# Kernel optimization log

Measured on AMD Instinct MI355X. Metric: run time of the kernel, lower is better.

The kernel has to match this reference:

```python
import jax, jax.numpy as jnp
import numpy as np

NUM_CAT = 16
SEG_LENS = np.array([4, 2, 2, 4, 4, 3, 3, 2, 4, 6, 2, 6, 3, 3, 3, 3], dtype=np.int64)
SHIFTS = np.concatenate([[0], np.cumsum(SEG_LENS)[:-1]]).astype(np.int64)
MAX_SEG_COUNT = int(SEG_LENS.max())           # 6
MAX_SEG = int(SHIFTS[-1] + SEG_LENS[-1] - 1)  # 53
IN = 128
N = 65536
EPS = 1e-5  # BatchNorm1d default eps
SLOPE = 0.2  # LeakyReLU negative slope


def setup_inputs() -> dict:
    key = jax.random.key(0)
    ks = jax.random.split(key, 4)
    features = jax.random.normal(ks[0], (N, IN), dtype=jnp.float32)
    category_labels = jax.random.randint(ks[1], (N,), 0, NUM_CAT, dtype=jnp.int64)
    # channel raising MLP: Linear(IN -> NUM_CAT*IN, bias=False)
    W1 = jax.random.normal(ks[2], (IN, NUM_CAT * IN), dtype=jnp.float32) * (1.0 / np.sqrt(IN))
    gamma = jnp.ones((NUM_CAT * IN,), dtype=jnp.float32)
    beta = jnp.zeros((NUM_CAT * IN,), dtype=jnp.float32)
    # UnaryConv weight: xavier_normal over (NUM_CAT, IN, MAX_SEG_COUNT)
    W2 = jax.random.normal(ks[3], (NUM_CAT, IN, MAX_SEG_COUNT), dtype=jnp.float32) * np.sqrt(2.0 / (IN + MAX_SEG_COUNT))
    bias = jnp.zeros((MAX_SEG_COUNT,), dtype=jnp.float32)
    return dict(features=features, W1=W1, gamma=gamma, beta=beta, W2=W2, bias=bias,
                category_labels=category_labels)


def reference(features, W1, gamma, beta, W2, bias, category_labels):
    n = features.shape[0]
    # channel raising: Linear -> BatchNorm1d (batch stats) -> LeakyReLU(0.2)
    h = features @ W1                                   # [N, C*D]
    mean = h.mean(axis=0)
    var = h.var(axis=0)                                 # biased, as in torch BN
    h = (h - mean) / jnp.sqrt(var + EPS) * gamma + beta
    h = jnp.where(h >= 0, h, SLOPE * h)
    # per-category batched matmul classifier
    h = h.reshape(n, NUM_CAT, IN).transpose(1, 0, 2)    # [C, N, D]
    logits_all = jnp.einsum('cnd,cds->cns', h, W2) + bias  # [C, N, S]
    n_idx = jnp.arange(n)
    logits = logits_all[category_labels, n_idx]         # gather: [N, S]
    logsm = jax.nn.log_softmax(logits, axis=-1)
    # scatter into per-category segment ranges of the [N, MAX_SEG+1] output
    shifts = jnp.asarray(SHIFTS)[category_labels]       # [N]
    seg_len = jnp.asarray(SEG_LENS)[category_labels]    # [N]
    s_idx = jnp.arange(MAX_SEG_COUNT)
    valid = s_idx[None, :] < seg_len[:, None]           # [N, S]
    cols = jnp.clip(shifts[:, None] + s_idx[None, :], 0, MAX_SEG)
    vals = jnp.where(valid, logsm, 0.0)                 # invalid slots add 0
    out = jnp.zeros((n, MAX_SEG + 1), dtype=logsm.dtype)
    out = out.at[n_idx[:, None], cols].add(vals)
    return out
```

## Files before the change

### kernel.cpp

```cpp
#include <hip/hip_runtime.h>
#include <hip/hip_bf16.h>

#define NCAT 16

typedef __attribute__((ext_vector_type(8))) short short8v;
typedef __attribute__((ext_vector_type(4))) float float4v;
typedef __attribute__((ext_vector_type(16))) float f32x16;

__constant__ int c_shift[NCAT] = {0,4,6,8,12,16,19,22,24,28,34,36,42,45,48,51};
__constant__ int c_len[NCAT]   = {4,2,2,4,4,3,3,2,4,6,2,6,3,3,3,3};


static inline __device__ unsigned pk2(float lo, float hi) {
  float2 f2; f2.x = lo; f2.y = hi;
  __hip_bfloat162 h = __float22bfloat162_rn(f2);
  unsigned u; __builtin_memcpy(&u, &h, 4);
  return u;
}
static inline __device__ float bf2f(unsigned short v) {
  unsigned u = (unsigned)v << 16;
  float f; __builtin_memcpy(&f, &u, 4);
  return f;
}

template<bool PART>
__global__ __launch_bounds__(1024) void k_stats_m(
    const float* __restrict__ F, const float* __restrict__ W1,
    const float* __restrict__ W2,
    float* __restrict__ Gdst, unsigned* __restrict__ Gp16,
    float* __restrict__ sv, float* __restrict__ svpart,
    unsigned short* __restrict__ Wlb, float* __restrict__ W2p)
{
  const int tid = threadIdx.x;
  if (blockIdx.x >= 256) {
    const int cat = (int)blockIdx.x - 256;
    for (int e = tid; e < 2048; e += 1024) {
      const int fid = e >> 6, l = e & 63;
      const int ks = fid >> 3, ct = fid & 7;
      const int kb = 32 * ks + 8 * (l >> 4);
      const int c = cat * 128 + 16 * ct + (l & 15);
      uint4 pk;
      pk.x = pk2(W1[(size_t)(kb + 0) * 2048 + c], W1[(size_t)(kb + 1) * 2048 + c]);
      pk.y = pk2(W1[(size_t)(kb + 2) * 2048 + c], W1[(size_t)(kb + 3) * 2048 + c]);
      pk.z = pk2(W1[(size_t)(kb + 4) * 2048 + c], W1[(size_t)(kb + 5) * 2048 + c]);
      pk.w = pk2(W1[(size_t)(kb + 6) * 2048 + c], W1[(size_t)(kb + 7) * 2048 + c]);
      *(uint4*)(Wlb + ((size_t)(cat * 32 + fid) * 64 + l) * 8) = pk;
    }
    if (tid < 1024) {
      const int c = tid >> 3, s = tid & 7;
      W2p[cat * 1024 + tid] = (s < 6) ? W2[cat * 768 + c * 6 + s] : 0.f;
    }
    return;
  }

  const int rowbase = blockIdx.x * 256;
  const int wid = tid >> 6, lane = tid & 63;
  const int wi = wid >> 2, wj = wid & 3;
  const int i0 = wi * 32, j0 = wj * 32;
  const int lr = lane & 31, lh = lane >> 5;

  f32x16 acc;
  #pragma unroll
  for (int e = 0; e < 16; ++e) acc[e] = 0.f;
  float svacc = 0.f;

  for (int ch = 0; ch < 8; ++ch) {
    #pragma unroll
    for (int h = 0; h < 2; ++h) {
      const int rbase = rowbase + ch * 32 + 16 * h + 8 * lh;
      float fa[8], fb[8];
      #pragma unroll
      for (int j = 0; j < 8; ++j) {
        const float* rp = F + (size_t)(rbase + j) * 128;
        fa[j] = rp[i0 + lr];
        fb[j] = rp[j0 + lr];
      }
      if (wj == 0) {
        #pragma unroll
        for (int j = 0; j < 8; ++j) svacc += fa[j];
      }
      uint4 av4, bv4;
      av4.x = pk2(fa[0], fa[1]); av4.y = pk2(fa[2], fa[3]);
      av4.z = pk2(fa[4], fa[5]); av4.w = pk2(fa[6], fa[7]);
      bv4.x = pk2(fb[0], fb[1]); bv4.y = pk2(fb[2], fb[3]);
      bv4.z = pk2(fb[4], fb[5]); bv4.w = pk2(fb[6], fb[7]);
      acc = __builtin_amdgcn_mfma_f32_32x32x16_bf16(
          __builtin_bit_cast(short8v, av4), __builtin_bit_cast(short8v, bv4),
          acc, 0, 0, 0);
    }
  }

  if (wj == 0) {
    svacc += __shfl_xor(svacc, 32);
    if (lane < 32) {
      if (PART) svpart[blockIdx.x * 128 + i0 + lr] = svacc;
      else      atomicAdd(&sv[i0 + lr], svacc);
    }
  }

  if (PART) {
    unsigned* gp = Gp16 + (size_t)blockIdx.x * 8192;
    #pragma unroll
    for (int t = 0; t < 8; ++t) {
      const int rowe = ((2 * t) & 3) + 8 * (t >> 1) + 4 * lh;
      gp[((i0 + rowe) >> 1) * 128 + j0 + lr] = pk2(acc[2 * t], acc[2 * t + 1]);
    }
  } else {
    #pragma unroll
    for (int reg = 0; reg < 16; ++reg) {
      const int row = (reg & 3) + 8 * (reg >> 2) + 4 * lh;
      atomicAdd(&Gdst[(i0 + row) * 128 + j0 + lr], acc[reg]);
    }
  }
}

__global__ __launch_bounds__(256) void k_reduce(
    const unsigned* __restrict__ Gp16, const float* __restrict__ svpart,
    float* __restrict__ G, float* __restrict__ sv)
{
  const int b = blockIdx.x, tid = threadIdx.x;
  if (b < 64) {
    const int e = b * 128 + (tid >> 1);
    const int half = tid & 1;
    float lo = 0.f, hi = 0.f;
    #pragma unroll 4
    for (int p = half * 128; p < half * 128 + 128; ++p) {
      const unsigned u = Gp16[(size_t)p * 8192 + e];
      lo += bf2f((unsigned short)(u & 0xffffu));
      hi += bf2f((unsigned short)(u >> 16));
    }
    lo += __shfl_xor(lo, 1);
    hi += __shfl_xor(hi, 1);
    if (half == 0) {
      const int pr = e >> 7, col = e & 127;
      G[(2 * pr) * 128 + col]     = lo;
      G[(2 * pr + 1) * 128 + col] = hi;
    }
  } else {
    if (tid < 128) {
      float s = 0.f;
      #pragma unroll 8
      for (int p = 0; p < 256; ++p) s += svpart[p * 128 + tid];
      sv[tid] = s;
    }
  }
}

__global__ __launch_bounds__(256) void k_params(
    const float* __restrict__ G, const float* __restrict__ sv,
    const float* __restrict__ W1, const float* __restrict__ gamma,
    const float* __restrict__ beta, float* __restrict__ scale,
    float* __restrict__ shiftv)
{
  __shared__ float Gl[128][133];
  __shared__ float Wl[128][16];
  __shared__ float redq[16][16];
  __shared__ float redm[16][16];
  const int tid = threadIdx.x;
  const int jb = blockIdx.x * 16;
  for (int i = tid; i < 16384; i += 256) Gl[i >> 7][i & 127] = G[i];
  for (int i = tid; i < 2048; i += 256) {
    int k = i >> 4, col = i & 15;
    Wl[k][col] = W1[(size_t)k * 2048 + jb + col];
  }
  __syncthreads();
  const int col = tid & 15, part = tid >> 4;
  float msq = 0.f, mean = 0.f;
  for (int ii = 0; ii < 8; ++ii) {
    const int i = part * 8 + ii;
    const float wi = Wl[i][col];
    float inner = 0.f;
    #pragma unroll 8
    for (int k = 0; k < 128; ++k) inner = fmaf(Gl[i][k], Wl[k][col], inner);
    msq = fmaf(wi, inner, msq);
  }
  #pragma unroll
  for (int kk = 0; kk < 8; ++kk) {
    const int k = part * 8 + kk;
    mean = fmaf(sv[k], Wl[k][col], mean);
  }
  redq[part][col] = msq;
  redm[part][col] = mean;
  __syncthreads();
  if (tid < 16) {
    float q = 0.f, m = 0.f;
    #pragma unroll
    for (int p = 0; p < 16; ++p) { q += redq[p][tid]; m += redm[p][tid]; }
    m *= (1.f / 65536.f);
    q *= (1.f / 65536.f);
    float var = q - m * m;
    float sc = gamma[jb + tid] * rsqrtf(var + 1e-5f);
    scale[jb + tid] = sc;
    shiftv[jb + tid] = beta[jb + tid] - m * sc;
  }
}

__global__ __launch_bounds__(512, 2) void k_main(
    const float* __restrict__ F, const unsigned short* __restrict__ Wlb,
    const float* __restrict__ W2p, const float* __restrict__ bias,
    const float* __restrict__ scale, const float* __restrict__ shiftv,
    const int* __restrict__ lab, float* __restrict__ out)
{
  __shared__ __attribute__((aligned(16))) unsigned short Fl[128 * 128];
  __shared__ __attribute__((aligned(16))) float obuf[128 * 54];
  __shared__ unsigned short lrows[128];
  __shared__ int wcs[2][NCAT];
  __shared__ int loff[NCAT + 1];
  __shared__ unsigned char gcat[32], gsub[32];
  __shared__ int gtot;

  const int tid = threadIdx.x;
  const int blk = (int)blockIdx.x;
  const int wid = tid >> 6, lane = tid & 63;
  const int lrow = lane & 15, lhi = lane >> 4;

  {
    for (int i = tid; i < 2048; i += 512) {
      const int r = i >> 4, cb = i & 15;
      const float4* src = (const float4*)(F + ((size_t)(blk * 128 + r)) * 128 + cb * 8);
      const float4 a0 = src[0];
      const float4 a1 = src[1];
      uint4 pk;
      pk.x = pk2(a0.x, a0.y); pk.y = pk2(a0.z, a0.w);
      pk.z = pk2(a1.x, a1.y); pk.w = pk2(a1.z, a1.w);
      const int co = (cb * 16) ^ ((r & 7) << 4);
      *(uint4*)((char*)Fl + r * 256 + co) = pk;
    }
    float4* ob4 = (float4*)obuf;
    for (int i = tid; i < 1728; i += 512) ob4[i] = make_float4(0.f, 0.f, 0.f, 0.f);
  }

  int myc = 0, myrank = 0;
  if (tid < 128) {
    myc = lab[blk * 128 + tid];
    const unsigned long long lanebit = 1ull << lane;
    #pragma unroll
    for (int cc = 0; cc < NCAT; ++cc) {
      unsigned long long m = __ballot(myc == cc);
      if (lane == 0) wcs[wid][cc] = (int)__popcll(m);
      if (myc == cc) myrank = (int)__popcll(m & (lanebit - 1));
    }
  }
  __syncthreads();
  if (tid == 0) {
    int a = 0, g = 0;
    for (int c = 0; c < NCAT; ++c) {
      loff[c] = a;
      const int cnt = wcs[0][c] + wcs[1][c];
      for (int s2 = 0; s2 * 16 < cnt; ++s2) {
        gcat[g] = (unsigned char)c; gsub[g] = (unsigned char)s2; ++g;
      }
      a += cnt;
    }
    loff[NCAT] = a;
    gtot = g;
  }
  __syncthreads();
  if (tid < 128) {
    const int wbase = (wid == 1) ? wcs[0][myc] : 0;
    lrows[loff[myc] + wbase + myrank] = (unsigned short)tid;
  }
  __syncthreads();

  float bi[6];
  #pragma unroll
  for (int s = 0; s < 6; ++s) bi[s] = bias[s];

  const int ng = gtot;
  for (int g = wid; g < ng; g += 8) {
    const int cat = gcat[g];
    const int slot0 = loff[cat] + ((int)gsub[g] << 4);
    const int hi2 = loff[cat + 1];
    const int navail = min(16, hi2 - slot0);
    const int srow = lrows[min(slot0 + lrow, hi2 - 1)];
    const unsigned short* wbase2 = Wlb + (size_t)cat * 16384;

    float4v acc[8];
    #pragma unroll
    for (int ct = 0; ct < 8; ++ct) acc[ct] = (float4v){0.f, 0.f, 0.f, 0.f};

    #pragma unroll
    for (int ks = 0; ks < 4; ++ks) {
      const int co = (ks * 64 + lhi * 16) ^ ((srow & 7) << 4);
      const short8v av = *(const short8v*)((const char*)Fl + srow * 256 + co);
      #pragma unroll
      for (int ct = 0; ct < 8; ++ct) {
        short8v bv = *(const short8v*)(wbase2 + ((ks * 8 + ct) * 64 + lane) * 8);
        acc[ct] = __builtin_amdgcn_mfma_f32_16x16x32_bf16(av, bv, acc[ct], 0, 0, 0);
      }
    }

    float p[4][6];
    #pragma unroll
    for (int j = 0; j < 4; ++j)
      #pragma unroll
      for (int s = 0; s < 6; ++s) p[j][s] = 0.f;
    #pragma unroll
    for (int ct = 0; ct < 8; ++ct) {
      const int c = ct * 16 + lrow;
      const float s_ = scale[cat * 128 + c];
      const float h_ = shiftv[cat * 128 + c];
      const float4* w2p4 = (const float4*)(W2p + ((size_t)cat * 128 + c) * 8);
      const float4 wa = w2p4[0];
      const float4 wb = w2p4[1];
      const float w2v[6] = {wa.x, wa.y, wa.z, wa.w, wb.x, wb.y};
      #pragma unroll
      for (int j = 0; j < 4; ++j) {
        float a = acc[ct][j] * s_ + h_;
        a = (a >= 0.f) ? a : 0.2f * a;
        #pragma unroll
        for (int s = 0; s < 6; ++s) p[j][s] = fmaf(a, w2v[s], p[j][s]);
      }
    }
    const bool b1 = (lrow & 1) != 0;
    const bool b2 = (lrow & 2) != 0;
    float q[2][6], r[6];
    #pragma unroll
    for (int t = 0; t < 2; ++t)
      #pragma unroll
      for (int s = 0; s < 6; ++s) {
        float snd = b1 ? p[2 * t][s] : p[2 * t + 1][s];
        float kp  = b1 ? p[2 * t + 1][s] : p[2 * t][s];
        q[t][s] = kp + __shfl_xor(snd, 1);
      }
    #pragma unroll
    for (int s = 0; s < 6; ++s) {
      float snd = b2 ? q[0][s] : q[1][s];
      float kp  = b2 ? q[1][s] : q[0][s];
      r[s] = kp + __shfl_xor(snd, 2);
    }
    #pragma unroll
    for (int s = 0; s < 6; ++s) r[s] += __shfl_xor(r[s], 4);
    #pragma unroll
    for (int s = 0; s < 6; ++s) r[s] += __shfl_xor(r[s], 8);

    const int jj = lrow & 3, sb = lrow >> 2;
    const int jrow = 4 * lhi + jj;
    float pj[6];
    #pragma unroll
    for (int s = 0; s < 6; ++s) pj[s] = r[s] + bi[s];
    float mx = fmaxf(fmaxf(fmaxf(pj[0], pj[1]), fmaxf(pj[2], pj[3])), fmaxf(pj[4], pj[5]));
    float e = __expf(pj[0] - mx) + __expf(pj[1] - mx) + __expf(pj[2] - mx)
            + __expf(pj[3] - mx) + __expf(pj[4] - mx) + __expf(pj[5] - mx);
    float lse = mx + __logf(e);

    if (jrow < navail) {
      const int orow = (int)lrows[slot0 + jrow];
      const int shc = c_shift[cat], lnc = c_len[cat];
      float* ob = obuf + orow * 54 + shc;
      if (sb == 0) {
        ob[0] = pj[0] - lse;
        ob[1] = pj[1] - lse;
        if (lnc > 2) ob[2] = pj[2] - lse;
        if (lnc > 3) ob[3] = pj[3] - lse;
      } else if (sb == 1) {
        if (lnc > 4) ob[4] = pj[4] - lse;
        if (lnc > 5) ob[5] = pj[5] - lse;
      }
    }
  }
  __syncthreads();

  {
    const float4* ob4 = (const float4*)obuf;
    float4* o4 = (float4*)(out + (size_t)blk * 6912);
    for (int i = tid; i < 1728; i += 512) o4[i] = ob4[i];
  }
}

extern "C" void kernel_launch(void* const* d_in, const int* in_sizes, int n_in,
                              void* d_out, int out_size, void* d_ws, size_t ws_size,
                              hipStream_t stream) {
  const float* F     = (const float*)d_in[0];
  const float* W1    = (const float*)d_in[1];
  const float* gamma = (const float*)d_in[2];
  const float* beta  = (const float*)d_in[3];
  const float* W2    = (const float*)d_in[4];
  const float* bias  = (const float*)d_in[5];
  const int*   lab   = (const int*)d_in[6];
  float* out = (float*)d_out;

  char* ws = (char*)d_ws;
  float* scale   = (float*)(ws + 0);
  float* shiftv  = (float*)(ws + 8192);
  float* G       = (float*)(ws + 16384);
  float* sv      = (float*)(ws + 81920);
  unsigned short* Wlb = (unsigned short*)(ws + 82432);
  float* W2p     = (float*)(ws + 606720);
  unsigned* Gp16 = (unsigned*)(ws + 672256);
  float* svpart  = (float*)(ws + 9060864);

  const size_t need = 9191936;
  if (ws_size >= need) {
    hipLaunchKernelGGL(k_stats_m<true>, dim3(272), dim3(1024), 0, stream,
                       F, W1, W2, G, Gp16, sv, svpart, Wlb, W2p);
    hipLaunchKernelGGL(k_reduce, dim3(65), dim3(256), 0, stream,
                       Gp16, svpart, G, sv);
  } else {
    hipMemsetAsync(ws + 16384, 0, 66048, stream);
    hipLaunchKernelGGL(k_stats_m<false>, dim3(272), dim3(1024), 0, stream,
                       F, W1, W2, G, Gp16, sv, svpart, Wlb, W2p);
  }
  hipLaunchKernelGGL(k_params, dim3(128), dim3(256), 0, stream,
                     G, sv, W1, gamma, beta, scale, shiftv);
  hipLaunchKernelGGL(k_main, dim3(512), dim3(512), 0, stream,
                     F, Wlb, W2p, bias, scale, shiftv, lab, out);
}
```

Baseline: 78.45 us.

## Software-pipeline W1 fragment loads across k-steps and groups in k_main

Double-buffers the per-category bf16 weight fragments in registers. The next k-step's fragments, and the next group's first k-step fragments, are loaded while the current MFMAs run. This hides global/L2 load latency behind MFMA work. Launch bounds drop from 2 to 1 blocks per SM to allow the extra registers, at the cost of lower occupancy and less latency hiding from concurrent waves.

```diff
diff --git a/kernel.cpp b/kernel.cpp
--- a/kernel.cpp
+++ b/kernel.cpp
@@ -195,7 +195,7 @@
   }
 }
 
-__global__ __launch_bounds__(512, 2) void k_main(
+__global__ __launch_bounds__(512, 1) void k_main(
     const float* __restrict__ F, const unsigned short* __restrict__ Wlb,
     const float* __restrict__ W2p, const float* __restrict__ bias,
     const float* __restrict__ scale, const float* __restrict__ shiftv,
@@ -267,95 +267,122 @@
   for (int s = 0; s < 6; ++s) bi[s] = bias[s];
 
   const int ng = gtot;
-  for (int g = wid; g < ng; g += 8) {
-    const int cat = gcat[g];
-    const int slot0 = loff[cat] + ((int)gsub[g] << 4);
-    const int hi2 = loff[cat + 1];
-    const int navail = min(16, hi2 - slot0);
-    const int srow = lrows[min(slot0 + lrow, hi2 - 1)];
-    const unsigned short* wbase2 = Wlb + (size_t)cat * 16384;
-
-    float4v acc[8];
-    #pragma unroll
-    for (int ct = 0; ct < 8; ++ct) acc[ct] = (float4v){0.f, 0.f, 0.f, 0.f};
-
-    #pragma unroll
-    for (int ks = 0; ks < 4; ++ks) {
-      const int co = (ks * 64 + lhi * 16) ^ ((srow & 7) << 4);
-      const short8v av = *(const short8v*)((const char*)Fl + srow * 256 + co);
+  if (wid < ng) {
+    int catc = gcat[wid];
+    int slot0c = loff[catc] + ((int)gsub[wid] << 4);
+    int hi2c = loff[catc + 1];
+    int srowc = lrows[min(slot0c + lrow, hi2c - 1)];
+    const short8v* wbc = (const short8v*)(Wlb + (size_t)catc * 16384);
+    short8v bcur[8], bnxt[8];
+    #pragma unroll
+    for (int ct = 0; ct < 8; ++ct) bcur[ct] = wbc[ct * 64 + lane];
+
+    for (int g = wid; g < ng; g += 8) {
+      const int cat = catc, slot0 = slot0c, srow = srowc;
+      const int navail = min(16, hi2c - slot0c);
+      const short8v* wb = wbc;
+
+      const int gn = g + 8;
+      const bool hn = gn < ng;
+      if (hn) {
+        catc = gcat[gn];
+        slot0c = loff[catc] + ((int)gsub[gn] << 4);
+        hi2c = loff[catc + 1];
+        srowc = lrows[min(slot0c + lrow, hi2c - 1)];
+        wbc = (const short8v*)(Wlb + (size_t)catc * 16384);
+      }
+
+      float4v acc[8];
+      #pragma unroll
+      for (int ct = 0; ct < 8; ++ct) acc[ct] = (float4v){0.f, 0.f, 0.f, 0.f};
+
+      #pragma unroll
+      for (int ks = 0; ks < 4; ++ks) {
+        if (ks < 3) {
+          #pragma unroll
+          for (int ct = 0; ct < 8; ++ct)
+            bnxt[ct] = wb[((ks + 1) * 8 + ct) * 64 + lane];
+        } else if (hn) {
+          #pragma unroll
+          for (int ct = 0; ct < 8; ++ct)
+            bnxt[ct] = wbc[ct * 64 + lane];
+        }
+        const int co = (ks * 64 + lhi * 16) ^ ((srow & 7) << 4);
+        const short8v av = *(const short8v*)((const char*)Fl + srow * 256 + co);
+        #pragma unroll
+        for (int ct = 0; ct < 8; ++ct)
+          acc[ct] = __builtin_amdgcn_mfma_f32_16x16x32_bf16(av, bcur[ct], acc[ct], 0, 0, 0);
+        #pragma unroll
+        for (int ct = 0; ct < 8; ++ct) bcur[ct] = bnxt[ct];
+      }
+
+      float p[4][6];
+      #pragma unroll
+      for (int j = 0; j < 4; ++j)
+        #pragma unroll
+        for (int s = 0; s < 6; ++s) p[j][s] = 0.f;
       #pragma unroll
       for (int ct = 0; ct < 8; ++ct) {
-        short8v bv = *(const short8v*)(wbase2 + ((ks * 8 + ct) * 64 + lane) * 8);
-        acc[ct] = __builtin_amdgcn_mfma_f32_16x16x32_bf16(av, bv, acc[ct], 0, 0, 0);
-      }
-    }
-
-    float p[4][6];
-    #pragma unroll
-    for (int j = 0; j < 4; ++j)
-      #pragma unroll
-      for (int s = 0; s < 6; ++s) p[j][s] = 0.f;
-    #pragma unroll
-    for (int ct = 0; ct < 8; ++ct) {
-      const int c = ct * 16 + lrow;
-      const float s_ = scale[cat * 128 + c];
-      const float h_ = shiftv[cat * 128 + c];
-      const float4* w2p4 = (const float4*)(W2p + ((size_t)cat * 128 + c) * 8);
-      const float4 wa = w2p4[0];
-      const float4 wb = w2p4[1];
-      const float w2v[6] = {wa.x, wa.y, wa.z, wa.w, wb.x, wb.y};
-      #pragma unroll
-      for (int j = 0; j < 4; ++j) {
-        float a = acc[ct][j] * s_ + h_;
-        a = (a >= 0.f) ? a : 0.2f * a;
-        #pragma unroll
-        for (int s = 0; s < 6; ++s) p[j][s] = fmaf(a, w2v[s], p[j][s]);
-      }
-    }
-    const bool b1 = (lrow & 1) != 0;
-    const bool b2 = (lrow & 2) != 0;
-    float q[2][6], r[6];
-    #pragma unroll
-    for (int t = 0; t < 2; ++t)
+        const int c = ct * 16 + lrow;
+        const float s_ = scale[cat * 128 + c];
+        const float h_ = shiftv[cat * 128 + c];
+        const float4* w2p4 = (const float4*)(W2p + ((size_t)cat * 128 + c) * 8);
+        const float4 wa = w2p4[0];
+        const float4 wb4 = w2p4[1];
+        const float w2v[6] = {wa.x, wa.y, wa.z, wa.w, wb4.x, wb4.y};
+        #pragma unroll
+        for (int j = 0; j < 4; ++j) {
+          float a = acc[ct][j] * s_ + h_;
+          a = (a >= 0.f) ? a : 0.2f * a;
+          #pragma unroll
+          for (int s = 0; s < 6; ++s) p[j][s] = fmaf(a, w2v[s], p[j][s]);
+        }
+      }
+      const bool b1 = (lrow & 1) != 0;
+      const bool b2 = (lrow & 2) != 0;
+      float q[2][6], r[6];
+      #pragma unroll
+      for (int t = 0; t < 2; ++t)
+        #pragma unroll
+        for (int s = 0; s < 6; ++s) {
+          float snd = b1 ? p[2 * t][s] : p[2 * t + 1][s];
+          float kp  = b1 ? p[2 * t + 1][s] : p[2 * t][s];
+          q[t][s] = kp + __shfl_xor(snd, 1);
+        }
       #pragma unroll
       for (int s = 0; s < 6; ++s) {
-        float snd = b1 ? p[2 * t][s] : p[2 * t + 1][s];
-        float kp  = b1 ? p[2 * t + 1][s] : p[2 * t][s];
-        q[t][s] = kp + __shfl_xor(snd, 1);
-      }
-    #pragma unroll
-    for (int s = 0; s < 6; ++s) {
-      float snd = b2 ? q[0][s] : q[1][s];
-      float kp  = b2 ? q[1][s] : q[0][s];
-      r[s] = kp + __shfl_xor(snd, 2);
-    }
-    #pragma unroll
-    for (int s = 0; s < 6; ++s) r[s] += __shfl_xor(r[s], 4);
-    #pragma unroll
-    for (int s = 0; s < 6; ++s) r[s] += __shfl_xor(r[s], 8);
-
-    const int jj = lrow & 3, sb = lrow >> 2;
-    const int jrow = 4 * lhi + jj;
-    float pj[6];
-    #pragma unroll
-    for (int s = 0; s < 6; ++s) pj[s] = r[s] + bi[s];
-    float mx = fmaxf(fmaxf(fmaxf(pj[0], pj[1]), fmaxf(pj[2], pj[3])), fmaxf(pj[4], pj[5]));
-    float e = __expf(pj[0] - mx) + __expf(pj[1] - mx) + __expf(pj[2] - mx)
-            + __expf(pj[3] - mx) + __expf(pj[4] - mx) + __expf(pj[5] - mx);
-    float lse = mx + __logf(e);
-
-    if (jrow < navail) {
-      const int orow = (int)lrows[slot0 + jrow];
-      const int shc = c_shift[cat], lnc = c_len[cat];
-      float* ob = obuf + orow * 54 + shc;
-      if (sb == 0) {
-        ob[0] = pj[0] - lse;
-        ob[1] = pj[1] - lse;
-        if (lnc > 2) ob[2] = pj[2] - lse;
-        if (lnc > 3) ob[3] = pj[3] - lse;
-      } else if (sb == 1) {
-        if (lnc > 4) ob[4] = pj[4] - lse;
-        if (lnc > 5) ob[5] = pj[5] - lse;
+        float snd = b2 ? q[0][s] : q[1][s];
+        float kp  = b2 ? q[1][s] : q[0][s];
+        r[s] = kp + __shfl_xor(snd, 2);
+      }
+      #pragma unroll
+      for (int s = 0; s < 6; ++s) r[s] += __shfl_xor(r[s], 4);
+      #pragma unroll
+      for (int s = 0; s < 6; ++s) r[s] += __shfl_xor(r[s], 8);
+
+      const int jj = lrow & 3, sb = lrow >> 2;
+      const int jrow = 4 * lhi + jj;
+      float pj[6];
+      #pragma unroll
+      for (int s = 0; s < 6; ++s) pj[s] = r[s] + bi[s];
+      float mx = fmaxf(fmaxf(fmaxf(pj[0], pj[1]), fmaxf(pj[2], pj[3])), fmaxf(pj[4], pj[5]));
+      float e = __expf(pj[0] - mx) + __expf(pj[1] - mx) + __expf(pj[2] - mx)
+              + __expf(pj[3] - mx) + __expf(pj[4] - mx) + __expf(pj[5] - mx);
+      float lse = mx + __logf(e);
+
+      if (jrow < navail) {
+        const int orow = (int)lrows[slot0 + jrow];
+        const int shc = c_shift[cat], lnc = c_len[cat];
+        float* ob = obuf + orow * 54 + shc;
+        if (sb == 0) {
+          ob[0] = pj[0] - lse;
+          ob[1] = pj[1] - lse;
+          if (lnc > 2) ob[2] = pj[2] - lse;
+          if (lnc > 3) ob[3] = pj[3] - lse;
+        } else if (sb == 1) {
+          if (lnc > 4) ob[4] = pj[4] - lse;
+          if (lnc > 5) ob[5] = pj[5] - lse;
+        }
       }
     }
   }
```

After: 77.98 us. No clear change (-0.6%).
